# Kernel tuning notes

Measured on AMD Instinct MI355X. Metric: run time of the kernel, lower is better.

## Reference

```python
import jax, jax.numpy as jnp
import numpy as np

NUM_USERS = 100000
NUM_ITEMS = 200000
D = 128          # embedding_dim
K = 4            # num interest heads
B = 4096
H = 256          # history length
H1, H2 = 512, 256  # hidden_units


def setup_inputs() -> dict:
    key = jax.random.key(0)
    ks = jax.random.split(key, 10)
    inp = {
        "user_ids": jax.random.randint(ks[0], (B,), 0, NUM_USERS),
        "candidate_items": jax.random.randint(ks[1], (B,), 0, NUM_ITEMS),
        "history_items": jax.random.randint(ks[2], (B, H), 0, NUM_ITEMS),
        "item_table": jax.random.normal(ks[3], (NUM_ITEMS, D), dtype=jnp.float32) * 0.05,
        "Wp": jax.random.normal(ks[4], (D, K), dtype=jnp.float32) * (1.0 / np.sqrt(D)),
        "W1": jax.random.normal(ks[5], (2 * D, H1), dtype=jnp.float32) * (1.0 / np.sqrt(2 * D)),
        "b1": jnp.zeros((H1,), dtype=jnp.float32),
        "W2": jax.random.normal(ks[6], (H1, H2), dtype=jnp.float32) * (1.0 / np.sqrt(H1)),
        "b2": jnp.zeros((H2,), dtype=jnp.float32),
        "W3": jax.random.normal(ks[7], (H2, 1), dtype=jnp.float32) * (1.0 / np.sqrt(H2)),
        "b3": jnp.zeros((1,), dtype=jnp.float32),
    }
    return inp


def reference(user_ids, candidate_items, history_items, item_table, Wp,
              W1, b1, W2, b2, W3, b3):
    # user_ids is unused by the original forward (user_emb never applied)
    item_vecs = item_table[history_items]          # (B, H, D)
    cand_vec = item_table[candidate_items]         # (B, D)

    # per-interest attention scores, softmax over history axis
    scores = jnp.einsum('bhd,dk->bhk', item_vecs, Wp)   # (B, H, K)
    scores = jax.nn.softmax(scores, axis=1)

    # softmax-weighted pooling -> K interest vectors per user
    interest_vectors = jnp.einsum('bhk,bhd->bkd', scores, item_vecs)  # (B, K, D)

    # similarity to candidate, pick best interest (data-dependent gather)
    sim_scores = jnp.einsum('bkd,bd->bk', interest_vectors, cand_vec)  # (B, K)
    best_idx = jnp.argmax(sim_scores, axis=-1)                          # (B,)
    selected = jnp.take_along_axis(
        interest_vectors, best_idx[:, None, None], axis=1)[:, 0, :]    # (B, D)

    # MLP tail: [2D -> 512] ReLU [512 -> 256] ReLU [256 -> 1], sigmoid
    x = jnp.concatenate([selected, cand_vec], axis=-1)  # (B, 2D)
    x = jax.nn.relu(x @ W1 + b1)
    x = jax.nn.relu(x @ W2 + b2)
    out = (x @ W3 + b3)[:, 0]                            # (B,)
    return jax.nn.sigmoid(out)
```

## Files before the change

### kernel.cpp

```cpp
#include <hip/hip_runtime.h>
#include <hip/hip_bf16.h>
#include <math.h>

#define B_SZ   4096
#define H_LEN  256
#define D_DIM  128
#define K_HEADS 4
#define H1_DIM 512
#define H2_DIM 256

#define CH     32
#define NCH    8
#define TPAD   132

typedef __attribute__((ext_vector_type(8))) short bf16x8;
typedef __attribute__((ext_vector_type(4))) float f32x4;

#define LDS_BARRIER() do {                                   \
    asm volatile("s_waitcnt lgkmcnt(0)" ::: "memory");       \
    __builtin_amdgcn_s_barrier();                            \
} while (0)

__global__ __launch_bounds__(256, 6) void interest_kernel(
    const int*   __restrict__ cand_ids,
    const int*   __restrict__ hist,
    const float* __restrict__ table,
    const float* __restrict__ Wp,
    __hip_bfloat16* __restrict__ Xbf)
{
    __shared__ float tile[CH * TPAD];
    __shared__ float wpt[K_HEADS * D_DIM];
    __shared__ float exps4[CH * 4];
    __shared__ float candv[D_DIM];
    __shared__ int   rowids[H_LEN];
    __shared__ float lsumW[16];
    __shared__ float simred[4][K_HEADS];
    __shared__ int   bestk;

    const int b    = blockIdx.x;
    const int t    = threadIdx.x;
    const int lane = t & 63, w = t >> 6;
    const int r    = t >> 3, q = t & 7;
    const int d    = t & 127, half = t >> 7;

    if (t < D_DIM) {
        float4 w4 = ((const float4*)Wp)[t];
        wpt[0 * D_DIM + t] = w4.x;
        wpt[1 * D_DIM + t] = w4.y;
        wpt[2 * D_DIM + t] = w4.z;
        wpt[3 * D_DIM + t] = w4.w;
    }
    const int cand = cand_ids[b];
    if (t >= 128 && t < 160) {
        int c = t - 128;
        ((float4*)candv)[c] = ((const float4*)(table + (long long)cand * D_DIM))[c];
    }
    rowids[t] = hist[(long long)b * H_LEN + t];

    float4 v0, v1, v2, v3;
    {
        const int row0 = hist[(long long)b * H_LEN + r];
        const float* rp = table + (long long)row0 * D_DIM + (q << 2);
        v0 = *(const float4*)(rp + 0 * 32);
        v1 = *(const float4*)(rp + 1 * 32);
        v2 = *(const float4*)(rp + 2 * 32);
        v3 = *(const float4*)(rp + 3 * 32);
    }

    LDS_BARRIER();

    float a0 = 0.f, a1 = 0.f, a2 = 0.f, a3 = 0.f;
    float l0 = 0.f, l1 = 0.f, l2 = 0.f, l3 = 0.f;

    for (int c = 0; c < NCH; ++c) {
        float4 u0, u1, u2, u3;
        if (c + 1 < NCH) {
            const int row = rowids[((c + 1) << 5) + r];
            const float* rp = table + (long long)row * D_DIM + (q << 2);
            u0 = *(const float4*)(rp + 0 * 32);
            u1 = *(const float4*)(rp + 1 * 32);
            u2 = *(const float4*)(rp + 2 * 32);
            u3 = *(const float4*)(rp + 3 * 32);
        }

        float s0 = 0.f, s1 = 0.f, s2 = 0.f, s3 = 0.f;
        float4 va;
        #define DO_J(JJ, VV)                                                    \
        {   va = VV;                                                            \
            const int cb = (q << 2) + (JJ << 5);                                \
            float4 w0 = *(const float4*)(wpt + 0 * D_DIM + cb);                 \
            float4 w1 = *(const float4*)(wpt + 1 * D_DIM + cb);                 \
            float4 w2 = *(const float4*)(wpt + 2 * D_DIM + cb);                 \
            float4 w3 = *(const float4*)(wpt + 3 * D_DIM + cb);                 \
            s0 += va.x * w0.x + va.y * w0.y + va.z * w0.z + va.w * w0.w;        \
            s1 += va.x * w1.x + va.y * w1.y + va.z * w1.z + va.w * w1.w;        \
            s2 += va.x * w2.x + va.y * w2.y + va.z * w2.z + va.w * w2.w;        \
            s3 += va.x * w3.x + va.y * w3.y + va.z * w3.z + va.w * w3.w;        \
            *(float4*)(tile + r * TPAD + cb) = va;                              \
        }
        DO_J(0, v0) DO_J(1, v1) DO_J(2, v2) DO_J(3, v3)
        #undef DO_J

        s0 += __shfl_xor(s0, 1); s0 += __shfl_xor(s0, 2); s0 += __shfl_xor(s0, 4);
        s1 += __shfl_xor(s1, 1); s1 += __shfl_xor(s1, 2); s1 += __shfl_xor(s1, 4);
        s2 += __shfl_xor(s2, 1); s2 += __shfl_xor(s2, 2); s2 += __shfl_xor(s2, 4);
        s3 += __shfl_xor(s3, 1); s3 += __shfl_xor(s3, 2); s3 += __shfl_xor(s3, 4);

        float e0 = expf(s0), e1 = expf(s1), e2 = expf(s2), e3 = expf(s3);
        if (q == 0) ((float4*)exps4)[r] = make_float4(e0, e1, e2, e3);

        float t0 = e0, t1 = e1, t2 = e2, t3 = e3;
        #pragma unroll
        for (int off = 8; off <= 32; off <<= 1) {
            t0 += __shfl_xor(t0, off);
            t1 += __shfl_xor(t1, off);
            t2 += __shfl_xor(t2, off);
            t3 += __shfl_xor(t3, off);
        }
        l0 += t0; l1 += t1; l2 += t2; l3 += t3;

        LDS_BARRIER();

        #pragma unroll
        for (int i = 0; i < 16; ++i) {
            int hl = (half << 4) + i;
            float4 e4 = ((const float4*)exps4)[hl];
            float  vv = tile[hl * TPAD + d];
            a0 += e4.x * vv; a1 += e4.y * vv; a2 += e4.z * vv; a3 += e4.w * vv;
        }

        LDS_BARRIER();

        if (c + 1 < NCH) { v0 = u0; v1 = u1; v2 = u2; v3 = u3; }
    }

    __syncthreads();
    float* partBp = tile;
    float* ivbufp = tile + 512;

    if (half == 1) ((float4*)partBp)[d] = make_float4(a0, a1, a2, a3);
    if (lane == 0) ((float4*)lsumW)[w]  = make_float4(l0, l1, l2, l3);
    __syncthreads();

    float s0 = 0.f, s1 = 0.f, s2 = 0.f, s3 = 0.f;
    if (half == 0) {
        float4 pb = ((const float4*)partBp)[d];
        float4 L0 = ((const float4*)lsumW)[0];
        float4 L1 = ((const float4*)lsumW)[1];
        float4 L2 = ((const float4*)lsumW)[2];
        float4 L3 = ((const float4*)lsumW)[3];
        float i0 = 1.f / (L0.x + L1.x + L2.x + L3.x);
        float i1 = 1.f / (L0.y + L1.y + L2.y + L3.y);
        float i2 = 1.f / (L0.z + L1.z + L2.z + L3.z);
        float i3 = 1.f / (L0.w + L1.w + L2.w + L3.w);
        a0 = (a0 + pb.x) * i0;
        a1 = (a1 + pb.y) * i1;
        a2 = (a2 + pb.z) * i2;
        a3 = (a3 + pb.w) * i3;
        ((float4*)ivbufp)[d] = make_float4(a0, a1, a2, a3);
        float cd = candv[d];
        s0 = a0 * cd; s1 = a1 * cd; s2 = a2 * cd; s3 = a3 * cd;
    }
    #pragma unroll
    for (int off = 32; off >= 1; off >>= 1) {
        s0 += __shfl_xor(s0, off);
        s1 += __shfl_xor(s1, off);
        s2 += __shfl_xor(s2, off);
        s3 += __shfl_xor(s3, off);
    }
    if (lane == 0) {
        simred[w][0] = s0; simred[w][1] = s1;
        simred[w][2] = s2; simred[w][3] = s3;
    }
    __syncthreads();

    if (t == 0) {
        float sim[4];
        #pragma unroll
        for (int k = 0; k < 4; ++k)
            sim[k] = simred[0][k] + simred[1][k] + simred[2][k] + simred[3][k];
        int best = 0;
        #pragma unroll
        for (int k = 1; k < 4; ++k) if (sim[k] > sim[best]) best = k;
        bestk = best;
    }
    __syncthreads();

    __hip_bfloat16* xrow = Xbf + (long long)b * (2 * D_DIM);
    if (t < 128) xrow[t] = __float2bfloat16(ivbufp[t * 4 + bestk]);
    else         xrow[t] = __float2bfloat16(candv[t - 128]);
}

__global__ __launch_bounds__(256) void convert_weights(
    const float* __restrict__ W1, const float* __restrict__ W2,
    __hip_bfloat16* __restrict__ W1t, __hip_bfloat16* __restrict__ W2t)
{
    __shared__ float tl[32][33];
    int bid = blockIdx.x;
    const float* W; __hip_bfloat16* Wt; int K, N;
    if (bid < 128) { W = W1; Wt = W1t; K = 2 * D_DIM; N = H1_DIM; }
    else           { W = W2; Wt = W2t; K = H1_DIM;    N = H2_DIM; bid -= 128; }
    const int ntn = N >> 5;
    const int k0 = (bid / ntn) << 5, n0 = (bid % ntn) << 5;
    const int tx = threadIdx.x & 31, ty = threadIdx.x >> 5;
    #pragma unroll
    for (int j = 0; j < 4; ++j)
        tl[ty + 8 * j][tx] = W[(long long)(k0 + ty + 8 * j) * N + n0 + tx];
    __syncthreads();
    #pragma unroll
    for (int j = 0; j < 4; ++j)
        Wt[(long long)(n0 + ty + 8 * j) * K + k0 + tx] =
            __float2bfloat16(tl[tx][ty + 8 * j]);
}

__global__ __launch_bounds__(512) void mlp_fused(
    const __hip_bfloat16* __restrict__ X,
    const __hip_bfloat16* __restrict__ W1t,
    const float* __restrict__ b1,
    const __hip_bfloat16* __restrict__ W2t,
    const float* __restrict__ b2,
    const float* __restrict__ W3,
    const float* __restrict__ b3,
    float*       __restrict__ out)
{
    __shared__ __hip_bfloat16 h1[16][H1_DIM + 8];
    __shared__ float          h2[16][H2_DIM + 4];

    const int t    = threadIdx.x;
    const int wave = t >> 6, lane = t & 63;
    const int lm   = lane & 15, quad = lane >> 4;
    const int m0   = blockIdx.x * 16;

    const __hip_bfloat16* Ap = X + (long long)(m0 + lm) * (2 * D_DIM) + quad * 8;
    bf16x8 af[8];
    #pragma unroll
    for (int it = 0; it < 8; ++it) af[it] = *(const bf16x8*)(Ap + it * 32);

    #pragma unroll
    for (int tn = 0; tn < 4; ++tn) {
        const int n0 = (wave * 4 + tn) * 16;
        const __hip_bfloat16* Bp = W1t + (long long)(n0 + lm) * (2 * D_DIM) + quad * 8;
        f32x4 acc = {0.f, 0.f, 0.f, 0.f};
        #pragma unroll
        for (int it = 0; it < 8; ++it) {
            bf16x8 bfr = *(const bf16x8*)(Bp + it * 32);
            acc = __builtin_amdgcn_mfma_f32_16x16x32_bf16(af[it], bfr, acc, 0, 0, 0);
        }
        const float bv = b1[n0 + lm];
        #pragma unroll
        for (int i = 0; i < 4; ++i)
            h1[quad * 4 + i][n0 + lm] = __float2bfloat16(fmaxf(acc[i] + bv, 0.f));
    }
    __syncthreads();

    bf16x8 a2[16];
    #pragma unroll
    for (int it = 0; it < 16; ++it)
        a2[it] = *(const bf16x8*)(&h1[lm][quad * 8 + it * 32]);

    #pragma unroll
    for (int tn = 0; tn < 2; ++tn) {
        const int n0 = (wave * 2 + tn) * 16;
        const __hip_bfloat16* Bp = W2t + (long long)(n0 + lm) * H1_DIM + quad * 8;
        f32x4 acc = {0.f, 0.f, 0.f, 0.f};
        #pragma unroll
        for (int it = 0; it < 16; ++it) {
            bf16x8 bfr = *(const bf16x8*)(Bp + it * 32);
            acc = __builtin_amdgcn_mfma_f32_16x16x32_bf16(a2[it], bfr, acc, 0, 0, 0);
        }
        const float bv = b2[n0 + lm];
        #pragma unroll
        for (int i = 0; i < 4; ++i)
            h2[quad * 4 + i][n0 + lm] = fmaxf(acc[i] + bv, 0.f);
    }
    __syncthreads();

    {
        const int row = t >> 5, c = (t & 31) * 8;
        float s = 0.f;
        #pragma unroll
        for (int j = 0; j < 8; ++j) s += h2[row][c + j] * W3[c + j];
        #pragma unroll
        for (int off = 1; off <= 16; off <<= 1) s += __shfl_xor(s, off);
        if ((lane & 31) == 0)
            out[m0 + row] = 1.f / (1.f + expf(-(s + b3[0])));
    }
}

extern "C" void kernel_launch(void* const* d_in, const int* in_sizes, int n_in,
                              void* d_out, int out_size, void* d_ws, size_t ws_size,
                              hipStream_t stream) {
    const int*   cand  = (const int*)  d_in[1];
    const int*   hist  = (const int*)  d_in[2];
    const float* table = (const float*)d_in[3];
    const float* Wp    = (const float*)d_in[4];
    const float* W1    = (const float*)d_in[5];
    const float* b1    = (const float*)d_in[6];
    const float* W2    = (const float*)d_in[7];
    const float* b2    = (const float*)d_in[8];
    const float* W3    = (const float*)d_in[9];
    const float* b3    = (const float*)d_in[10];
    float* out = (float*)d_out;

    char* p = (char*)d_ws;
    __hip_bfloat16* Xbf = (__hip_bfloat16*)p;  p += (size_t)B_SZ * 2 * D_DIM * 2;
    __hip_bfloat16* W1t = (__hip_bfloat16*)p;  p += (size_t)H1_DIM * 2 * D_DIM * 2;
    __hip_bfloat16* W2t = (__hip_bfloat16*)p;

    convert_weights<<<256, 256, 0, stream>>>(W1, W2, W1t, W2t);
    interest_kernel<<<B_SZ, 256, 0, stream>>>(cand, hist, table, Wp, Xbf);
    mlp_fused<<<B_SZ / 16, 512, 0, stream>>>(Xbf, W1t, b1, W2t, b2, W3, b3, out);
}
```

Before: 260.8 us.

## Gather history rows from a per-call bf16 copy of the item table

Each call now converts the whole fp32 item table to bf16 inside a merged conversion kernel. The interest kernel then gathers 16-byte bf16x8 vectors instead of fp32, with 64-row chunks and lower occupancy bounds. This halves the bytes moved by the random history gather, but adds a full read and write of the table each call and lowers embedding precision. The MLP kernel is also changed to 1024 threads, with one W2 tile per wave and a per-wave final dot product. The old fp32 path is kept as a fallback when the workspace is too small.

```diff
diff --git a/kernel.cpp b/kernel.cpp
--- a/kernel.cpp
+++ b/kernel.cpp
@@ -8,9 +8,10 @@
 #define K_HEADS 4
 #define H1_DIM 512
 #define H2_DIM 256
-
-#define CH     32
-#define NCH    8
+#define NUM_ITEMS 200000
+
+#define CH     64
+#define NCH    4
 #define TPAD   132
 
 typedef __attribute__((ext_vector_type(8))) short bf16x8;
@@ -21,10 +22,16 @@
     __builtin_amdgcn_s_barrier();                            \
 } while (0)
 
-__global__ __launch_bounds__(256, 6) void interest_kernel(
+__device__ __forceinline__ float bf2f(short s) {
+    unsigned u = ((unsigned)(unsigned short)s) << 16;
+    float f; __builtin_memcpy(&f, &u, 4); return f;
+}
+
+__global__ __launch_bounds__(256, 4) void interest_kernel_bf16(
     const int*   __restrict__ cand_ids,
     const int*   __restrict__ hist,
     const float* __restrict__ table,
+    const __hip_bfloat16* __restrict__ tableB,
     const float* __restrict__ Wp,
     __hip_bfloat16* __restrict__ Xbf)
 {
@@ -40,7 +47,7 @@
     const int b    = blockIdx.x;
     const int t    = threadIdx.x;
     const int lane = t & 63, w = t >> 6;
-    const int r    = t >> 3, q = t & 7;
+    const int r    = t >> 2, q = t & 3;
     const int d    = t & 127, half = t >> 7;
 
     if (t < D_DIM) {
@@ -57,14 +64,14 @@
     }
     rowids[t] = hist[(long long)b * H_LEN + t];
 
-    float4 v0, v1, v2, v3;
+    bf16x8 v0, v1, v2, v3;
     {
         const int row0 = hist[(long long)b * H_LEN + r];
-        const float* rp = table + (long long)row0 * D_DIM + (q << 2);
-        v0 = *(const float4*)(rp + 0 * 32);
-        v1 = *(const float4*)(rp + 1 * 32);
-        v2 = *(const float4*)(rp + 2 * 32);
-        v3 = *(const float4*)(rp + 3 * 32);
+        const __hip_bfloat16* rp = tableB + (long long)row0 * D_DIM + (q << 3);
+        v0 = *(const bf16x8*)(rp + 0 * 32);
+        v1 = *(const bf16x8*)(rp + 1 * 32);
+        v2 = *(const bf16x8*)(rp + 2 * 32);
+        v3 = *(const bf16x8*)(rp + 3 * 32);
     }
 
     LDS_BARRIER();
@@ -73,45 +80,57 @@
     float l0 = 0.f, l1 = 0.f, l2 = 0.f, l3 = 0.f;
 
     for (int c = 0; c < NCH; ++c) {
-        float4 u0, u1, u2, u3;
+        bf16x8 u0, u1, u2, u3;
         if (c + 1 < NCH) {
-            const int row = rowids[((c + 1) << 5) + r];
-            const float* rp = table + (long long)row * D_DIM + (q << 2);
-            u0 = *(const float4*)(rp + 0 * 32);
-            u1 = *(const float4*)(rp + 1 * 32);
-            u2 = *(const float4*)(rp + 2 * 32);
-            u3 = *(const float4*)(rp + 3 * 32);
+            const int row = rowids[((c + 1) << 6) + r];
+            const __hip_bfloat16* rp = tableB + (long long)row * D_DIM + (q << 3);
+            u0 = *(const bf16x8*)(rp + 0 * 32);
+            u1 = *(const bf16x8*)(rp + 1 * 32);
+            u2 = *(const bf16x8*)(rp + 2 * 32);
+            u3 = *(const bf16x8*)(rp + 3 * 32);
         }
 
         float s0 = 0.f, s1 = 0.f, s2 = 0.f, s3 = 0.f;
-        float4 va;
         #define DO_J(JJ, VV)                                                    \
-        {   va = VV;                                                            \
-            const int cb = (q << 2) + (JJ << 5);                                \
-            float4 w0 = *(const float4*)(wpt + 0 * D_DIM + cb);                 \
-            float4 w1 = *(const float4*)(wpt + 1 * D_DIM + cb);                 \
-            float4 w2 = *(const float4*)(wpt + 2 * D_DIM + cb);                 \
-            float4 w3 = *(const float4*)(wpt + 3 * D_DIM + cb);                 \
-            s0 += va.x * w0.x + va.y * w0.y + va.z * w0.z + va.w * w0.w;        \
-            s1 += va.x * w1.x + va.y * w1.y + va.z * w1.z + va.w * w1.w;        \
-            s2 += va.x * w2.x + va.y * w2.y + va.z * w2.z + va.w * w2.w;        \
-            s3 += va.x * w3.x + va.y * w3.y + va.z * w3.z + va.w * w3.w;        \
-            *(float4*)(tile + r * TPAD + cb) = va;                              \
+        {   const int cb = (q << 3) + (JJ << 5);                                \
+            float f0 = bf2f(VV[0]), f1 = bf2f(VV[1]);                           \
+            float f2 = bf2f(VV[2]), f3 = bf2f(VV[3]);                           \
+            float f4 = bf2f(VV[4]), f5 = bf2f(VV[5]);                           \
+            float f6 = bf2f(VV[6]), f7 = bf2f(VV[7]);                           \
+            float4 wA, wB;                                                      \
+            wA = *(const float4*)(wpt + 0 * D_DIM + cb);                        \
+            wB = *(const float4*)(wpt + 0 * D_DIM + cb + 4);                    \
+            s0 += f0*wA.x + f1*wA.y + f2*wA.z + f3*wA.w                         \
+                + f4*wB.x + f5*wB.y + f6*wB.z + f7*wB.w;                        \
+            wA = *(const float4*)(wpt + 1 * D_DIM + cb);                        \
+            wB = *(const float4*)(wpt + 1 * D_DIM + cb + 4);                    \
+            s1 += f0*wA.x + f1*wA.y + f2*wA.z + f3*wA.w                         \
+                + f4*wB.x + f5*wB.y + f6*wB.z + f7*wB.w;                        \
+            wA = *(const float4*)(wpt + 2 * D_DIM + cb);                        \
+            wB = *(const float4*)(wpt + 2 * D_DIM + cb + 4);                    \
+            s2 += f0*wA.x + f1*wA.y + f2*wA.z + f3*wA.w                         \
+                + f4*wB.x + f5*wB.y + f6*wB.z + f7*wB.w;                        \
+            wA = *(const float4*)(wpt + 3 * D_DIM + cb);                        \
+            wB = *(const float4*)(wpt + 3 * D_DIM + cb + 4);                    \
+            s3 += f0*wA.x + f1*wA.y + f2*wA.z + f3*wA.w                         \
+                + f4*wB.x + f5*wB.y + f6*wB.z + f7*wB.w;                        \
+            *(float4*)(tile + r * TPAD + cb)     = make_float4(f0, f1, f2, f3); \
+            *(float4*)(tile + r * TPAD + cb + 4) = make_float4(f4, f5, f6, f7); \
         }
         DO_J(0, v0) DO_J(1, v1) DO_J(2, v2) DO_J(3, v3)
         #undef DO_J
 
-        s0 += __shfl_xor(s0, 1); s0 += __shfl_xor(s0, 2); s0 += __shfl_xor(s0, 4);
-        s1 += __shfl_xor(s1, 1); s1 += __shfl_xor(s1, 2); s1 += __shfl_xor(s1, 4);
-        s2 += __shfl_xor(s2, 1); s2 += __shfl_xor(s2, 2); s2 += __shfl_xor(s2, 4);
-        s3 += __shfl_xor(s3, 1); s3 += __shfl_xor(s3, 2); s3 += __shfl_xor(s3, 4);
+        s0 += __shfl_xor(s0, 1); s0 += __shfl_xor(s0, 2);
+        s1 += __shfl_xor(s1, 1); s1 += __shfl_xor(s1, 2);
+        s2 += __shfl_xor(s2, 1); s2 += __shfl_xor(s2, 2);
+        s3 += __shfl_xor(s3, 1); s3 += __shfl_xor(s3, 2);
 
         float e0 = expf(s0), e1 = expf(s1), e2 = expf(s2), e3 = expf(s3);
         if (q == 0) ((float4*)exps4)[r] = make_float4(e0, e1, e2, e3);
 
         float t0 = e0, t1 = e1, t2 = e2, t3 = e3;
         #pragma unroll
-        for (int off = 8; off <= 32; off <<= 1) {
+        for (int off = 4; off <= 32; off <<= 1) {
             t0 += __shfl_xor(t0, off);
             t1 += __shfl_xor(t1, off);
             t2 += __shfl_xor(t2, off);
@@ -121,9 +140,9 @@
 
         LDS_BARRIER();
 
-        #pragma unroll
-        for (int i = 0; i < 16; ++i) {
-            int hl = (half << 4) + i;
+        #pragma unroll 8
+        for (int i = 0; i < 32; ++i) {
+            int hl = (half << 5) + i;
             float4 e4 = ((const float4*)exps4)[hl];
             float  vv = tile[hl * TPAD + d];
             a0 += e4.x * vv; a1 += e4.y * vv; a2 += e4.z * vv; a3 += e4.w * vv;
@@ -191,6 +210,193 @@
     else         xrow[t] = __float2bfloat16(candv[t - 128]);
 }
 
+__global__ __launch_bounds__(256, 6) void interest_kernel_f32(
+    const int*   __restrict__ cand_ids, const int* __restrict__ hist,
+    const float* __restrict__ table, const float* __restrict__ Wp,
+    __hip_bfloat16* __restrict__ Xbf)
+{
+    __shared__ float tile[32 * TPAD];
+    __shared__ float wpt[K_HEADS * D_DIM];
+    __shared__ float exps4[32 * 4];
+    __shared__ float candv[D_DIM];
+    __shared__ int   rowids[H_LEN];
+    __shared__ float lsumW[16];
+    __shared__ float simred[4][K_HEADS];
+    __shared__ int   bestk;
+
+    const int b    = blockIdx.x;
+    const int t    = threadIdx.x;
+    const int lane = t & 63, w = t >> 6;
+    const int r    = t >> 3, q = t & 7;
+    const int d    = t & 127, half = t >> 7;
+
+    if (t < D_DIM) {
+        float4 w4 = ((const float4*)Wp)[t];
+        wpt[0 * D_DIM + t] = w4.x; wpt[1 * D_DIM + t] = w4.y;
+        wpt[2 * D_DIM + t] = w4.z; wpt[3 * D_DIM + t] = w4.w;
+    }
+    const int cand = cand_ids[b];
+    if (t >= 128 && t < 160) {
+        int c = t - 128;
+        ((float4*)candv)[c] = ((const float4*)(table + (long long)cand * D_DIM))[c];
+    }
+    rowids[t] = hist[(long long)b * H_LEN + t];
+
+    float4 v0, v1, v2, v3;
+    {
+        const int row0 = hist[(long long)b * H_LEN + r];
+        const float* rp = table + (long long)row0 * D_DIM + (q << 2);
+        v0 = *(const float4*)(rp + 0 * 32); v1 = *(const float4*)(rp + 1 * 32);
+        v2 = *(const float4*)(rp + 2 * 32); v3 = *(const float4*)(rp + 3 * 32);
+    }
+    LDS_BARRIER();
+
+    float a0 = 0.f, a1 = 0.f, a2 = 0.f, a3 = 0.f;
+    float l0 = 0.f, l1 = 0.f, l2 = 0.f, l3 = 0.f;
+
+    for (int c = 0; c < 8; ++c) {
+        float4 u0, u1, u2, u3;
+        if (c + 1 < 8) {
+            const int row = rowids[((c + 1) << 5) + r];
+            const float* rp = table + (long long)row * D_DIM + (q << 2);
+            u0 = *(const float4*)(rp + 0 * 32); u1 = *(const float4*)(rp + 1 * 32);
+            u2 = *(const float4*)(rp + 2 * 32); u3 = *(const float4*)(rp + 3 * 32);
+        }
+        float s0 = 0.f, s1 = 0.f, s2 = 0.f, s3 = 0.f;
+        float4 va;
+        #define DO_J(JJ, VV)                                                    \
+        {   va = VV;                                                            \
+            const int cb = (q << 2) + (JJ << 5);                                \
+            float4 w0 = *(const float4*)(wpt + 0 * D_DIM + cb);                 \
+            float4 w1 = *(const float4*)(wpt + 1 * D_DIM + cb);                 \
+            float4 w2 = *(const float4*)(wpt + 2 * D_DIM + cb);                 \
+            float4 w3 = *(const float4*)(wpt + 3 * D_DIM + cb);                 \
+            s0 += va.x*w0.x + va.y*w0.y + va.z*w0.z + va.w*w0.w;                \
+            s1 += va.x*w1.x + va.y*w1.y + va.z*w1.z + va.w*w1.w;                \
+            s2 += va.x*w2.x + va.y*w2.y + va.z*w2.z + va.w*w2.w;                \
+            s3 += va.x*w3.x + va.y*w3.y + va.z*w3.z + va.w*w3.w;                \
+            *(float4*)(tile + r * TPAD + cb) = va;                              \
+        }
+        DO_J(0, v0) DO_J(1, v1) DO_J(2, v2) DO_J(3, v3)
+        #undef DO_J
+
+        s0 += __shfl_xor(s0, 1); s0 += __shfl_xor(s0, 2); s0 += __shfl_xor(s0, 4);
+        s1 += __shfl_xor(s1, 1); s1 += __shfl_xor(s1, 2); s1 += __shfl_xor(s1, 4);
+        s2 += __shfl_xor(s2, 1); s2 += __shfl_xor(s2, 2); s2 += __shfl_xor(s2, 4);
+        s3 += __shfl_xor(s3, 1); s3 += __shfl_xor(s3, 2); s3 += __shfl_xor(s3, 4);
+
+        float e0 = expf(s0), e1 = expf(s1), e2 = expf(s2), e3 = expf(s3);
+        if (q == 0) ((float4*)exps4)[r] = make_float4(e0, e1, e2, e3);
+
+        float t0 = e0, t1 = e1, t2 = e2, t3 = e3;
+        #pragma unroll
+        for (int off = 8; off <= 32; off <<= 1) {
+            t0 += __shfl_xor(t0, off); t1 += __shfl_xor(t1, off);
+            t2 += __shfl_xor(t2, off); t3 += __shfl_xor(t3, off);
+        }
+        l0 += t0; l1 += t1; l2 += t2; l3 += t3;
+
+        LDS_BARRIER();
+        #pragma unroll
+        for (int i = 0; i < 16; ++i) {
+            int hl = (half << 4) + i;
+            float4 e4 = ((const float4*)exps4)[hl];
+            float  vv = tile[hl * TPAD + d];
+            a0 += e4.x * vv; a1 += e4.y * vv; a2 += e4.z * vv; a3 += e4.w * vv;
+        }
+        LDS_BARRIER();
+        if (c + 1 < 8) { v0 = u0; v1 = u1; v2 = u2; v3 = u3; }
+    }
+
+    __syncthreads();
+    float* partBp = tile;
+    float* ivbufp = tile + 512;
+
+    if (half == 1) ((float4*)partBp)[d] = make_float4(a0, a1, a2, a3);
+    if (lane == 0) ((float4*)lsumW)[w]  = make_float4(l0, l1, l2, l3);
+    __syncthreads();
+
+    float s0 = 0.f, s1 = 0.f, s2 = 0.f, s3 = 0.f;
+    if (half == 0) {
+        float4 pb = ((const float4*)partBp)[d];
+        float4 L0 = ((const float4*)lsumW)[0];
+        float4 L1 = ((const float4*)lsumW)[1];
+        float4 L2 = ((const float4*)lsumW)[2];
+        float4 L3 = ((const float4*)lsumW)[3];
+        float i0 = 1.f / (L0.x + L1.x + L2.x + L3.x);
+        float i1 = 1.f / (L0.y + L1.y + L2.y + L3.y);
+        float i2 = 1.f / (L0.z + L1.z + L2.z + L3.z);
+        float i3 = 1.f / (L0.w + L1.w + L2.w + L3.w);
+        a0 = (a0 + pb.x) * i0; a1 = (a1 + pb.y) * i1;
+        a2 = (a2 + pb.z) * i2; a3 = (a3 + pb.w) * i3;
+        ((float4*)ivbufp)[d] = make_float4(a0, a1, a2, a3);
+        float cd = candv[d];
+        s0 = a0 * cd; s1 = a1 * cd; s2 = a2 * cd; s3 = a3 * cd;
+    }
+    #pragma unroll
+    for (int off = 32; off >= 1; off >>= 1) {
+        s0 += __shfl_xor(s0, off); s1 += __shfl_xor(s1, off);
+        s2 += __shfl_xor(s2, off); s3 += __shfl_xor(s3, off);
+    }
+    if (lane == 0) {
+        simred[w][0] = s0; simred[w][1] = s1;
+        simred[w][2] = s2; simred[w][3] = s3;
+    }
+    __syncthreads();
+    if (t == 0) {
+        float sim[4];
+        #pragma unroll
+        for (int k = 0; k < 4; ++k)
+            sim[k] = simred[0][k] + simred[1][k] + simred[2][k] + simred[3][k];
+        int best = 0;
+        #pragma unroll
+        for (int k = 1; k < 4; ++k) if (sim[k] > sim[best]) best = k;
+        bestk = best;
+    }
+    __syncthreads();
+
+    __hip_bfloat16* xrow = Xbf + (long long)b * (2 * D_DIM);
+    if (t < 128) xrow[t] = __float2bfloat16(ivbufp[t * 4 + bestk]);
+    else         xrow[t] = __float2bfloat16(candv[t - 128]);
+}
+
+__global__ __launch_bounds__(256) void convert_all(
+    const float* __restrict__ table,
+    const float* __restrict__ W1, const float* __restrict__ W2,
+    __hip_bfloat16* __restrict__ tableB,
+    __hip_bfloat16* __restrict__ W1t, __hip_bfloat16* __restrict__ W2t)
+{
+    __shared__ float tl[32][33];
+    int bid = blockIdx.x;
+    if (bid < 12500) {
+        long long idx = (long long)bid * 256 + threadIdx.x;
+        const float4* s = (const float4*)table + idx * 2;
+        float4 s0 = s[0], s1 = s[1];
+        __hip_bfloat16 o[8];
+        o[0] = __float2bfloat16(s0.x); o[1] = __float2bfloat16(s0.y);
+        o[2] = __float2bfloat16(s0.z); o[3] = __float2bfloat16(s0.w);
+        o[4] = __float2bfloat16(s1.x); o[5] = __float2bfloat16(s1.y);
+        o[6] = __float2bfloat16(s1.z); o[7] = __float2bfloat16(s1.w);
+        *(uint4*)(tableB + idx * 8) = *(uint4*)o;
+        return;
+    }
+    bid -= 12500;
+    const float* W; __hip_bfloat16* Wt; int K, N;
+    if (bid < 128) { W = W1; Wt = W1t; K = 2 * D_DIM; N = H1_DIM; }
+    else           { W = W2; Wt = W2t; K = H1_DIM;    N = H2_DIM; bid -= 128; }
+    const int ntn = N >> 5;
+    const int k0 = (bid / ntn) << 5, n0 = (bid % ntn) << 5;
+    const int tx = threadIdx.x & 31, ty = threadIdx.x >> 5;
+    #pragma unroll
+    for (int j = 0; j < 4; ++j)
+        tl[ty + 8 * j][tx] = W[(long long)(k0 + ty + 8 * j) * N + n0 + tx];
+    __syncthreads();
+    #pragma unroll
+    for (int j = 0; j < 4; ++j)
+        Wt[(long long)(n0 + ty + 8 * j) * K + k0 + tx] =
+            __float2bfloat16(tl[tx][ty + 8 * j]);
+}
+
 __global__ __launch_bounds__(256) void convert_weights(
     const float* __restrict__ W1, const float* __restrict__ W2,
     __hip_bfloat16* __restrict__ W1t, __hip_bfloat16* __restrict__ W2t)
@@ -213,7 +419,7 @@
             __float2bfloat16(tl[tx][ty + 8 * j]);
 }
 
-__global__ __launch_bounds__(512) void mlp_fused(
+__global__ __launch_bounds__(1024) void mlp_fused(
     const __hip_bfloat16* __restrict__ X,
     const __hip_bfloat16* __restrict__ W1t,
     const float* __restrict__ b1,
@@ -237,8 +443,8 @@
     for (int it = 0; it < 8; ++it) af[it] = *(const bf16x8*)(Ap + it * 32);
 
     #pragma unroll
-    for (int tn = 0; tn < 4; ++tn) {
-        const int n0 = (wave * 4 + tn) * 16;
+    for (int tn = 0; tn < 2; ++tn) {
+        const int n0 = (wave * 2 + tn) * 16;
         const __hip_bfloat16* Bp = W1t + (long long)(n0 + lm) * (2 * D_DIM) + quad * 8;
         f32x4 acc = {0.f, 0.f, 0.f, 0.f};
         #pragma unroll
@@ -253,20 +459,15 @@
     }
     __syncthreads();
 
-    bf16x8 a2[16];
-    #pragma unroll
-    for (int it = 0; it < 16; ++it)
-        a2[it] = *(const bf16x8*)(&h1[lm][quad * 8 + it * 32]);
-
-    #pragma unroll
-    for (int tn = 0; tn < 2; ++tn) {
-        const int n0 = (wave * 2 + tn) * 16;
+    {
+        const int n0 = wave * 16;
         const __hip_bfloat16* Bp = W2t + (long long)(n0 + lm) * H1_DIM + quad * 8;
         f32x4 acc = {0.f, 0.f, 0.f, 0.f};
         #pragma unroll
         for (int it = 0; it < 16; ++it) {
+            bf16x8 a2  = *(const bf16x8*)(&h1[lm][quad * 8 + it * 32]);
             bf16x8 bfr = *(const bf16x8*)(Bp + it * 32);
-            acc = __builtin_amdgcn_mfma_f32_16x16x32_bf16(a2[it], bfr, acc, 0, 0, 0);
+            acc = __builtin_amdgcn_mfma_f32_16x16x32_bf16(a2, bfr, acc, 0, 0, 0);
         }
         const float bv = b2[n0 + lm];
         #pragma unroll
@@ -276,13 +477,13 @@
     __syncthreads();
 
     {
-        const int row = t >> 5, c = (t & 31) * 8;
-        float s = 0.f;
-        #pragma unroll
-        for (int j = 0; j < 8; ++j) s += h2[row][c + j] * W3[c + j];
-        #pragma unroll
-        for (int off = 1; off <= 16; off <<= 1) s += __shfl_xor(s, off);
-        if ((lane & 31) == 0)
+        const int row = wave;
+        float4 hv = *(const float4*)(&h2[row][lane * 4]);
+        float4 w4 = ((const float4*)W3)[lane];
+        float s = hv.x * w4.x + hv.y * w4.y + hv.z * w4.z + hv.w * w4.w;
+        #pragma unroll
+        for (int off = 1; off <= 32; off <<= 1) s += __shfl_xor(s, off);
+        if (lane == 0)
             out[m0 + row] = 1.f / (1.f + expf(-(s + b3[0])));
     }
 }
@@ -305,9 +506,16 @@
     char* p = (char*)d_ws;
     __hip_bfloat16* Xbf = (__hip_bfloat16*)p;  p += (size_t)B_SZ * 2 * D_DIM * 2;
     __hip_bfloat16* W1t = (__hip_bfloat16*)p;  p += (size_t)H1_DIM * 2 * D_DIM * 2;
-    __hip_bfloat16* W2t = (__hip_bfloat16*)p;
-
-    convert_weights<<<256, 256, 0, stream>>>(W1, W2, W1t, W2t);
-    interest_kernel<<<B_SZ, 256, 0, stream>>>(cand, hist, table, Wp, Xbf);
-    mlp_fused<<<B_SZ / 16, 512, 0, stream>>>(Xbf, W1t, b1, W2t, b2, W3, b3, out);
-}
+    __hip_bfloat16* W2t = (__hip_bfloat16*)p;  p += (size_t)H1_DIM * H2_DIM * 2;
+    __hip_bfloat16* tableB = (__hip_bfloat16*)p;
+    const size_t need = ((char*)tableB - (char*)d_ws) + (size_t)NUM_ITEMS * D_DIM * 2;
+
+    if (ws_size >= need) {
+        convert_all<<<12500 + 256, 256, 0, stream>>>(table, W1, W2, tableB, W1t, W2t);
+        interest_kernel_bf16<<<B_SZ, 256, 0, stream>>>(cand, hist, table, tableB, Wp, Xbf);
+    } else {
+        convert_weights<<<256, 256, 0, stream>>>(W1, W2, W1t, W2t);
+        interest_kernel_f32<<<B_SZ, 256, 0, stream>>>(cand, hist, table, Wp, Xbf);
+    }
+    mlp_fused<<<B_SZ / 16, 1024, 0, stream>>>(Xbf, W1t, b1, W2t, b2, W3, b3, out);
+}
```

Measured after the change: 275.7 us. 5.7% more time.
